# Kernel optimization log

Measured on AMD Instinct MI355X. Metric: run time of the kernel, lower is better.

## Reference

```python
import jax, jax.numpy as jnp
import numpy as np

D = 768
H = 8
HD = D // H  # 96
DFF = 2048
EPS = 1e-5


def layernorm(x, g, b):
    mu = jnp.mean(x, axis=-1, keepdims=True)
    var = jnp.var(x, axis=-1, keepdims=True)
    return (x - mu) * jax.lax.rsqrt(var + EPS) * g + b


def setup_inputs() -> dict:
    key = jax.random.key(0)
    ks = jax.random.split(key, 12)
    B, L = 4, 1024
    s = lambda fan: 1.0 / np.sqrt(fan)
    return {
        "x": jax.random.normal(ks[0], (B, L, D), jnp.float32),
        "attn_bias": jax.random.normal(ks[1], (B, L, L), jnp.float32),
        "in_proj_w": jax.random.normal(ks[2], (3 * D, D), jnp.float32) * s(D),
        "in_proj_b": jnp.zeros((3 * D,), jnp.float32),
        "out_w": jax.random.normal(ks[3], (D, D), jnp.float32) * s(D),
        "out_b": jnp.zeros((D,), jnp.float32),
        "ff1_w": jax.random.normal(ks[4], (DFF, D), jnp.float32) * s(D),
        "ff1_b": jnp.zeros((DFF,), jnp.float32),
        "ff2_w": jax.random.normal(ks[5], (D, DFF), jnp.float32) * s(DFF),
        "ff2_b": jnp.zeros((D,), jnp.float32),
        "ln1_g": jnp.ones((D,), jnp.float32),
        "ln1_b": jnp.zeros((D,), jnp.float32),
        "ln2_g": jnp.ones((D,), jnp.float32),
        "ln2_b": jnp.zeros((D,), jnp.float32),
    }


def reference(x, attn_bias, in_proj_w, in_proj_b, out_w, out_b,
              ff1_w, ff1_b, ff2_w, ff2_b, ln1_g, ln1_b, ln2_g, ln2_b):
    B, L, _ = x.shape
    # combined QKV projection (torch nn.MultiheadAttention in_proj)
    qkv = x @ in_proj_w.T + in_proj_b  # [B,L,3D]
    q, k, v = jnp.split(qkv, 3, axis=-1)
    q = q.reshape(B, L, H, HD).transpose(0, 2, 1, 3)  # [B,H,L,hd]
    k = k.reshape(B, L, H, HD).transpose(0, 2, 1, 3)
    v = v.reshape(B, L, H, HD).transpose(0, 2, 1, 3)
    scale = 1.0 / np.sqrt(HD)
    scores = jnp.einsum('bhld,bhmd->bhlm', q, k) * scale + attn_bias[:, None, :, :]
    probs = jax.nn.softmax(scores, axis=-1)
    attn = jnp.einsum('bhlm,bhmd->bhld', probs, v)  # [B,H,L,hd]
    attn = attn.transpose(0, 2, 1, 3).reshape(B, L, D)
    attn = attn @ out_w.T + out_b
    x = layernorm(x + attn, ln1_g, ln1_b)
    h = jax.nn.gelu(x @ ff1_w.T + ff1_b, approximate=False) @ ff2_w.T + ff2_b
    x = layernorm(x + h, ln2_g, ln2_b)
    return x
```

## Files before the change

kernel.cpp:

```cpp
#include <hip/hip_runtime.h>

typedef __bf16 bf16x8 __attribute__((ext_vector_type(8)));
typedef float f32x4 __attribute__((ext_vector_type(4)));
typedef unsigned short u16x8 __attribute__((ext_vector_type(8)));
typedef short s16x4 __attribute__((ext_vector_type(4)));

__device__ __forceinline__ unsigned short f2b(float f) {
    union { float f; unsigned u; } v; v.f = f;
    unsigned r = (v.u + 0x7fffu + ((v.u >> 16) & 1u)) >> 16;
    return (unsigned short)r;
}

__device__ __forceinline__ void load_lds16(const void* g, void* l) {
    __builtin_amdgcn_global_load_lds(
        (const __attribute__((address_space(1))) unsigned int*)g,
        (__attribute__((address_space(3))) unsigned int*)l,
        16, 0, 0);
}

__global__ void cvt_kernel(const float* __restrict__ in, unsigned short* __restrict__ out, int n4) {
    int i = blockIdx.x * 256 + threadIdx.x;
    if (i < n4) {
        f32x4 v = ((const f32x4*)in)[i];
        s16x4 o;
        o.x = (short)f2b(v.x);
        o.y = (short)f2b(v.y);
        o.z = (short)f2b(v.z);
        o.w = (short)f2b(v.w);
        ((s16x4*)out)[i] = o;
    }
}

template <int BM, int BN, int EPI>
__global__ __launch_bounds__(512, 1)
void gemm_pipe(const unsigned short* __restrict__ A, const unsigned short* __restrict__ Bm,
               const float* __restrict__ bias, void* __restrict__ Cout,
               int M, int N, int K) {
    constexpr int ACH = BM / 8;
    constexpr int TC  = (BM + BN) / 8;
    constexpr int CPW = TC / 8;
    constexpr int MR = 4;
    constexpr int NR = BN / 64;
    constexpr int WN = BN / 4;
    constexpr int WSTR = (WN == 64) ? 72 : 36;
    constexpr int ABYTES = BM * 128;
    constexpr int BBYTES = BN * 128;
    constexpr int SMEM_BYTES = 3 * (ABYTES + BBYTES);
    static_assert(8 * 64 * WSTR * 4 <= SMEM_BYTES, "epilogue fits");
    __shared__ char smem[SMEM_BYTES];

    const int tid = threadIdx.x, lane = tid & 63, wid = tid >> 6;
    const int l15 = lane & 15, lq = lane >> 4;
    const int wr = wid >> 2, wc = wid & 3;

    const int nwg = gridDim.x * gridDim.y;
    int bid = blockIdx.y * gridDim.x + blockIdx.x;
    bid = (bid & 7) * (nwg >> 3) + (bid >> 3);
    const int bx = bid % gridDim.x, by = bid / gridDim.x;
    const int m0 = by * BM, n0 = bx * BN;

    const int srow = lane >> 3;
    const int scol = ((lane & 7) ^ srow) * 8;

    f32x4 acc[MR][NR];
#pragma unroll
    for (int i = 0; i < MR; i++)
#pragma unroll
        for (int j = 0; j < NR; j++) acc[i][j] = 0.0f;

    auto stage = [&](int buf, int kt) {
        const int kb = kt * 64;
#pragma unroll
        for (int i = 0; i < CPW; ++i) {
            const int c = wid * CPW + i;
            if (c < ACH) {
                load_lds16(A + (size_t)(m0 + c * 8 + srow) * K + kb + scol,
                           smem + buf * ABYTES + c * 1024);
            } else {
                load_lds16(Bm + (size_t)(n0 + (c - ACH) * 8 + srow) * K + kb + scol,
                           smem + 3 * ABYTES + buf * BBYTES + (c - ACH) * 1024);
            }
        }
    };

    auto compute = [&](int buf) {
#pragma unroll
        for (int kc = 0; kc < 2; ++kc) {
            const int cb = kc * 64;
            const int sw = (l15 & 7) << 4;
            bf16x8 af[MR], bf[NR];
#pragma unroll
            for (int mi = 0; mi < MR; mi++) {
                const int row = wr * 64 + mi * 16 + l15;
                af[mi] = *(const bf16x8*)(smem + buf * ABYTES + row * 128 + ((cb + lq * 16) ^ sw));
            }
#pragma unroll
            for (int ni = 0; ni < NR; ni++) {
                const int row = wc * WN + ni * 16 + l15;
                bf[ni] = *(const bf16x8*)(smem + 3 * ABYTES + buf * BBYTES + row * 128 + ((cb + lq * 16) ^ sw));
            }
#pragma unroll
            for (int mi = 0; mi < MR; mi++)
#pragma unroll
                for (int ni = 0; ni < NR; ni++)
                    acc[mi][ni] = __builtin_amdgcn_mfma_f32_16x16x32_bf16(af[mi], bf[ni], acc[mi][ni], 0, 0, 0);
        }
    };

    const int nkt = K / 64;
    stage(0, 0);
    stage(1, 1);
    stage(2, 2);
    int cur = 0;
    for (int t = 0; t < nkt; ++t) {
        if (t <= nkt - 3)      asm volatile("s_waitcnt vmcnt(12)" ::: "memory");
        else if (t == nkt - 2) asm volatile("s_waitcnt vmcnt(6)" ::: "memory");
        else                   asm volatile("s_waitcnt vmcnt(0)" ::: "memory");
        __builtin_amdgcn_s_barrier();
        asm volatile("" ::: "memory");
        compute(cur);
        asm volatile("" ::: "memory");
        __builtin_amdgcn_s_barrier();
        if (t + 3 < nkt) stage(cur, t + 3);
        cur = (cur == 2) ? 0 : cur + 1;
    }

    float* ew = (float*)(smem + wid * 64 * WSTR * 4);
#pragma unroll
    for (int mi = 0; mi < MR; mi++) {
#pragma unroll
        for (int ni = 0; ni < NR; ni++) {
            const int cl = ni * 16 + l15;
            const float bv = bias[n0 + wc * WN + cl];
#pragma unroll
            for (int r = 0; r < 4; r++) {
                const int rl = mi * 16 + lq * 4 + r;
                float v = acc[mi][ni][r] + bv;
                if constexpr (EPI == 2) {
                    v = 0.5f * v * (1.0f + erff(v * 0.7071067811865475f));
                }
                ew[rl * WSTR + (cl ^ (lq << 3))] = v;
            }
        }
    }
    asm volatile("s_waitcnt lgkmcnt(0)" ::: "memory");

    if constexpr (WN == 64) {
        const int r8 = lane >> 3, c8 = lane & 7;
#pragma unroll
        for (int j = 0; j < 8; j++) {
            const int row = r8 + 8 * j;
            const int po = c8 ^ ((row >> 2) & 3);
            f32x4 a = *(const f32x4*)(ew + row * WSTR + po * 8);
            f32x4 b = *(const f32x4*)(ew + row * WSTR + po * 8 + 4);
            const int grow = m0 + wr * 64 + row;
            const int gcol = n0 + wc * WN + c8 * 8;
            if constexpr (EPI == 1) {
                *(f32x4*)&((float*)Cout)[(size_t)grow * N + gcol] = a;
                *(f32x4*)&((float*)Cout)[(size_t)grow * N + gcol + 4] = b;
            } else {
                u16x8 p;
#pragma unroll
                for (int e = 0; e < 4; e++) { p[e] = f2b(a[e]); p[e + 4] = f2b(b[e]); }
                *(u16x8*)&((unsigned short*)Cout)[(size_t)grow * N + gcol] = p;
            }
        }
    } else {
        const int r8 = lane >> 2, c8 = lane & 3;
#pragma unroll
        for (int j = 0; j < 4; j++) {
            const int row = r8 + 16 * j;
            const int po = c8 ^ ((row >> 2) & 3);
            f32x4 a = *(const f32x4*)(ew + row * WSTR + po * 8);
            f32x4 b = *(const f32x4*)(ew + row * WSTR + po * 8 + 4);
            const int grow = m0 + wr * 64 + row;
            const int gcol = n0 + wc * WN + c8 * 8;
            if constexpr (EPI == 1) {
                *(f32x4*)&((float*)Cout)[(size_t)grow * N + gcol] = a;
                *(f32x4*)&((float*)Cout)[(size_t)grow * N + gcol + 4] = b;
            } else {
                u16x8 p;
#pragma unroll
                for (int e = 0; e < 4; e++) { p[e] = f2b(a[e]); p[e + 4] = f2b(b[e]); }
                *(u16x8*)&((unsigned short*)Cout)[(size_t)grow * N + gcol] = p;
            }
        }
    }
}

__global__ __launch_bounds__(256, 2)
void attn_kernel(const unsigned short* __restrict__ qkv,
                 const float* __restrict__ bias,
                 unsigned short* __restrict__ out) {
    const int L = 1024, TD = 2304, HD = 96;
    const int qt = blockIdx.x, h = blockIdx.y, b = blockIdx.z;
    const int tid = threadIdx.x, lane = tid & 63, wid = tid >> 6;
    const int l15 = lane & 15, lq = lane >> 4;
    const int q0 = qt * 64;
    const float scale = 0.10206207261596576f;

    __shared__ unsigned short Ks[64][104];
    __shared__ unsigned short Vt[96][72];
    __shared__ unsigned short Ps[4][16][72];
    __shared__ float Ot[4][16][100];

    bf16x8 qf[3];
    const int qrow = q0 + wid * 16 + l15;
#pragma unroll
    for (int kc = 0; kc < 3; kc++)
        qf[kc] = *(const bf16x8*)(qkv + (size_t)(b * L + qrow) * TD + h * HD + kc * 32 + lq * 8);

    f32x4 o[6];
#pragma unroll
    for (int df = 0; df < 6; df++) o[df] = 0.0f;
    float mrow[4] = {-1e30f, -1e30f, -1e30f, -1e30f};
    float lrow[4] = {0.f, 0.f, 0.f, 0.f};

    for (int kv0 = 0; kv0 < L; kv0 += 64) {
#pragma unroll
        for (int i = 0; i < 3; i++) {
            int c = i * 256 + tid;
            int row = c / 12, cc = c % 12;
            *(f32x4*)&Ks[row][cc * 8] =
                *(const f32x4*)(qkv + (size_t)(b * L + kv0 + row) * TD + 768 + h * HD + cc * 8);
        }
#pragma unroll
        for (int i = 0; i < 3; i++) {
            int dblk = i * 4 + wid;
            int m = lane;
            u16x8 v = *(const u16x8*)(qkv + (size_t)(b * L + kv0 + m) * TD + 1536 + h * HD + dblk * 8);
#pragma unroll
            for (int j = 0; j < 8; j++) Vt[dblk * 8 + j][m] = v[j];
        }
        __syncthreads();

        f32x4 s[4];
#pragma unroll
        for (int nf = 0; nf < 4; nf++) s[nf] = 0.0f;
#pragma unroll
        for (int kc = 0; kc < 3; kc++) {
#pragma unroll
            for (int nf = 0; nf < 4; nf++) {
                bf16x8 kf = *(const bf16x8*)&Ks[nf * 16 + l15][kc * 32 + lq * 8];
                s[nf] = __builtin_amdgcn_mfma_f32_16x16x32_bf16(qf[kc], kf, s[nf], 0, 0, 0);
            }
        }
#pragma unroll
        for (int nf = 0; nf < 4; nf++) {
            int colg = kv0 + nf * 16 + l15;
#pragma unroll
            for (int r = 0; r < 4; r++) {
                int rowg = q0 + wid * 16 + lq * 4 + r;
                s[nf][r] = s[nf][r] * scale + bias[((size_t)b * L + rowg) * L + colg];
            }
        }
        float pm[4];
#pragma unroll
        for (int r = 0; r < 4; r++) {
            float mx = fmaxf(fmaxf(s[0][r], s[1][r]), fmaxf(s[2][r], s[3][r]));
#pragma unroll
            for (int d = 1; d < 16; d <<= 1) mx = fmaxf(mx, __shfl_xor(mx, d, 64));
            pm[r] = mx;
        }
        float alpha[4];
#pragma unroll
        for (int r = 0; r < 4; r++) {
            float mn = fmaxf(mrow[r], pm[r]);
            alpha[r] = __expf(mrow[r] - mn);
            mrow[r] = mn;
        }
        float rs[4] = {0.f, 0.f, 0.f, 0.f};
#pragma unroll
        for (int nf = 0; nf < 4; nf++)
#pragma unroll
            for (int r = 0; r < 4; r++) {
                float p = __expf(s[nf][r] - mrow[r]);
                s[nf][r] = p;
                rs[r] += p;
            }
#pragma unroll
        for (int r = 0; r < 4; r++) {
#pragma unroll
            for (int d = 1; d < 16; d <<= 1) rs[r] += __shfl_xor(rs[r], d, 64);
            lrow[r] = lrow[r] * alpha[r] + rs[r];
        }
#pragma unroll
        for (int nf = 0; nf < 4; nf++)
#pragma unroll
            for (int r = 0; r < 4; r++)
                Ps[wid][lq * 4 + r][nf * 16 + l15] = f2b(s[nf][r]);
#pragma unroll
        for (int df = 0; df < 6; df++)
#pragma unroll
            for (int r = 0; r < 4; r++) o[df][r] *= alpha[r];
        asm volatile("s_waitcnt lgkmcnt(0)" ::: "memory");
#pragma unroll
        for (int kc = 0; kc < 2; kc++) {
            bf16x8 pf = *(const bf16x8*)&Ps[wid][l15][kc * 32 + lq * 8];
#pragma unroll
            for (int df = 0; df < 6; df++) {
                bf16x8 vf = *(const bf16x8*)&Vt[df * 16 + l15][kc * 32 + lq * 8];
                o[df] = __builtin_amdgcn_mfma_f32_16x16x32_bf16(pf, vf, o[df], 0, 0, 0);
            }
        }
        __syncthreads();
    }

#pragma unroll
    for (int r = 0; r < 4; r++) {
        float inv = 1.0f / lrow[r];
        const int rl = lq * 4 + r;
#pragma unroll
        for (int df = 0; df < 6; df++) {
            const int cl = df * 16 + l15;
            Ot[wid][rl][cl ^ (lq << 3)] = o[df][r] * inv;
        }
    }
    asm volatile("s_waitcnt lgkmcnt(0)" ::: "memory");
    {
        const int r = lane >> 2, c8 = lane & 3;
        const int rowg = q0 + wid * 16 + r;
#pragma unroll
        for (int it = 0; it < 3; it++) {
            const int oc = c8 + 4 * it;
            const int po = oc ^ ((r >> 2) & 3);
            f32x4 a = *(const f32x4*)&Ot[wid][r][po * 8];
            f32x4 bb = *(const f32x4*)&Ot[wid][r][po * 8 + 4];
            u16x8 p;
#pragma unroll
            for (int e = 0; e < 4; e++) { p[e] = f2b(a[e]); p[e + 4] = f2b(bb[e]); }
            *(u16x8*)&out[((size_t)b * L + rowg) * 768 + h * 96 + oc * 8] = p;
        }
    }
}

template <int WRITE_B>
__global__ __launch_bounds__(256, 4)
void ln_kernel(const float* __restrict__ x, const float* __restrict__ res,
               const float* __restrict__ g, const float* __restrict__ bvec,
               float* __restrict__ outf, unsigned short* __restrict__ outb) {
    const int Dm = 768;
    int row = blockIdx.x;
    int tid = threadIdx.x;
    f32x4 v = {0.f, 0.f, 0.f, 0.f};
    float sum = 0.f, sq = 0.f;
    if (tid < 192) {
        f32x4 xv = ((const f32x4*)(x + (size_t)row * Dm))[tid];
        f32x4 rv = ((const f32x4*)(res + (size_t)row * Dm))[tid];
        v = xv + rv;
        sum = v.x + v.y + v.z + v.w;
        sq = v.x * v.x + v.y * v.y + v.z * v.z + v.w * v.w;
    }
#pragma unroll
    for (int d = 1; d < 64; d <<= 1) {
        sum += __shfl_xor(sum, d, 64);
        sq += __shfl_xor(sq, d, 64);
    }
    __shared__ float ps[8];
    int lane = tid & 63, wid = tid >> 6;
    if (lane == 0) { ps[wid] = sum; ps[wid + 4] = sq; }
    __syncthreads();
    sum = ps[0] + ps[1] + ps[2] + ps[3];
    sq = ps[4] + ps[5] + ps[6] + ps[7];
    float mu = sum * (1.0f / 768.0f);
    float var = sq * (1.0f / 768.0f) - mu * mu;
    float rsg = rsqrtf(var + 1e-5f);
    if (tid < 192) {
        f32x4 gv = ((const f32x4*)g)[tid];
        f32x4 bv = ((const f32x4*)bvec)[tid];
        f32x4 ov;
#pragma unroll
        for (int e = 0; e < 4; e++) ov[e] = (v[e] - mu) * rsg * gv[e] + bv[e];
        ((f32x4*)(outf + (size_t)row * Dm))[tid] = ov;
        if constexpr (WRITE_B) {
            s16x4 pb;
#pragma unroll
            for (int e = 0; e < 4; e++) pb[e] = (short)f2b(ov[e]);
            ((s16x4*)(outb + (size_t)row * Dm))[tid] = pb;
        }
    }
}

extern "C" void kernel_launch(void* const* d_in, const int* in_sizes, int n_in,
                              void* d_out, int out_size, void* d_ws, size_t ws_size,
                              hipStream_t stream) {
    (void)in_sizes; (void)n_in; (void)out_size; (void)ws_size;
    const float* x         = (const float*)d_in[0];
    const float* attn_bias = (const float*)d_in[1];
    const float* in_proj_w = (const float*)d_in[2];
    const float* in_proj_b = (const float*)d_in[3];
    const float* out_w     = (const float*)d_in[4];
    const float* out_b     = (const float*)d_in[5];
    const float* ff1_w     = (const float*)d_in[6];
    const float* ff1_b     = (const float*)d_in[7];
    const float* ff2_w     = (const float*)d_in[8];
    const float* ff2_b     = (const float*)d_in[9];
    const float* ln1_g     = (const float*)d_in[10];
    const float* ln1_b     = (const float*)d_in[11];
    const float* ln2_g     = (const float*)d_in[12];
    const float* ln2_b     = (const float*)d_in[13];

    const int NTOK = 4096;
    char* ws = (char*)d_ws;
    size_t off = 0;
    auto alloc = [&](size_t bytes) { void* p = ws + off; off += (bytes + 255) & ~(size_t)255; return p; };
    unsigned short* xb    = (unsigned short*)alloc((size_t)NTOK * 768 * 2);
    unsigned short* wqkv  = (unsigned short*)alloc((size_t)2304 * 768 * 2);
    unsigned short* wout  = (unsigned short*)alloc((size_t)768 * 768 * 2);
    unsigned short* wff1  = (unsigned short*)alloc((size_t)2048 * 768 * 2);
    unsigned short* wff2  = (unsigned short*)alloc((size_t)768 * 2048 * 2);
    unsigned short* qkvb  = (unsigned short*)alloc((size_t)NTOK * 2304 * 2);
    unsigned short* attnb = (unsigned short*)alloc((size_t)NTOK * 768 * 2);
    float*          aproj = (float*)alloc((size_t)NTOK * 768 * 4);
    float*          x1f   = (float*)alloc((size_t)NTOK * 768 * 4);
    unsigned short* x1b   = (unsigned short*)alloc((size_t)NTOK * 768 * 2);
    unsigned short* h1b  = qkvb;
    float*          ff2o = aproj;

    cvt_kernel<<<dim3((NTOK * 768 / 4) / 256), 256, 0, stream>>>(x, xb, NTOK * 768 / 4);
    cvt_kernel<<<dim3((2304 * 768 / 4) / 256), 256, 0, stream>>>(in_proj_w, wqkv, 2304 * 768 / 4);
    cvt_kernel<<<dim3((768 * 768 / 4) / 256), 256, 0, stream>>>(out_w, wout, 768 * 768 / 4);
    cvt_kernel<<<dim3((2048 * 768 / 4) / 256), 256, 0, stream>>>(ff1_w, wff1, 2048 * 768 / 4);
    cvt_kernel<<<dim3((768 * 2048 / 4) / 256), 256, 0, stream>>>(ff2_w, wff2, 768 * 2048 / 4);

    gemm_pipe<128, 256, 0><<<dim3(2304 / 256, NTOK / 128), 512, 0, stream>>>(xb, wqkv, in_proj_b, qkvb, NTOK, 2304, 768);
    attn_kernel<<<dim3(16, 8, 4), 256, 0, stream>>>(qkvb, attn_bias, attnb);
    gemm_pipe<128, 128, 1><<<dim3(768 / 128, NTOK / 128), 512, 0, stream>>>(attnb, wout, out_b, aproj, NTOK, 768, 768);
    ln_kernel<1><<<dim3(NTOK), 256, 0, stream>>>(x, aproj, ln1_g, ln1_b, x1f, x1b);
    gemm_pipe<128, 256, 2><<<dim3(2048 / 256, NTOK / 128), 512, 0, stream>>>(x1b, wff1, ff1_b, h1b, NTOK, 2048, 768);
    gemm_pipe<128, 128, 1><<<dim3(768 / 128, NTOK / 128), 512, 0, stream>>>(h1b, wff2, ff2_b, ff2o, NTOK, 768, 2048);
    ln_kernel<0><<<dim3(NTOK), 256, 0, stream>>>(x1f, ff2o, ln2_g, ln2_b, (float*)d_out, nullptr);
}
```

Before: 180.7 us.

## Interleave GEMM global-to-LDS staging with MFMA phases and fuse conversion kernels

Result: no change. 183.8 us (+1.7%).

```diff
diff --git a/kernel.cpp b/kernel.cpp
--- a/kernel.cpp
+++ b/kernel.cpp
@@ -18,30 +18,49 @@
         16, 0, 0);
 }
 
-__global__ void cvt_kernel(const float* __restrict__ in, unsigned short* __restrict__ out, int n4) {
+template <int N> __device__ __forceinline__ void wait_vmcnt() {
+    if constexpr (N == 0)      asm volatile("s_waitcnt vmcnt(0)" ::: "memory");
+    else if constexpr (N == 4) asm volatile("s_waitcnt vmcnt(4)" ::: "memory");
+    else if constexpr (N == 6) asm volatile("s_waitcnt vmcnt(6)" ::: "memory");
+    else static_assert(N == 0 || N == 4 || N == 6, "unsupported vmcnt");
+}
+
+__global__ void cvt5_kernel(const float* __restrict__ s0, const float* __restrict__ s1,
+                            const float* __restrict__ s2, const float* __restrict__ s3,
+                            const float* __restrict__ s4,
+                            unsigned short* __restrict__ d0, unsigned short* __restrict__ d1,
+                            unsigned short* __restrict__ d2, unsigned short* __restrict__ d3,
+                            unsigned short* __restrict__ d4) {
     int i = blockIdx.x * 256 + threadIdx.x;
-    if (i < n4) {
-        f32x4 v = ((const f32x4*)in)[i];
-        s16x4 o;
-        o.x = (short)f2b(v.x);
-        o.y = (short)f2b(v.y);
-        o.z = (short)f2b(v.z);
-        o.w = (short)f2b(v.w);
-        ((s16x4*)out)[i] = o;
-    }
-}
-
-template <int BM, int BN, int EPI>
+    const float* s; unsigned short* d; int off;
+    if (i < 786432)       { s = s0; d = d0; off = 0; }
+    else if (i < 1228800) { s = s1; d = d1; off = 786432; }
+    else if (i < 1376256) { s = s2; d = d2; off = 1228800; }
+    else if (i < 1769472) { s = s3; d = d3; off = 1376256; }
+    else                  { s = s4; d = d4; off = 1769472; }
+    i -= off;
+    f32x4 v = ((const f32x4*)s)[i];
+    s16x4 o;
+    o.x = (short)f2b(v.x);
+    o.y = (short)f2b(v.y);
+    o.z = (short)f2b(v.z);
+    o.w = (short)f2b(v.w);
+    ((s16x4*)d)[i] = o;
+}
+
+template <int BN, int EPI>
 __global__ __launch_bounds__(512, 1)
-void gemm_pipe(const unsigned short* __restrict__ A, const unsigned short* __restrict__ Bm,
-               const float* __restrict__ bias, void* __restrict__ Cout,
-               int M, int N, int K) {
+void gemm_8ph(const unsigned short* __restrict__ A, const unsigned short* __restrict__ Bm,
+              const float* __restrict__ bias, void* __restrict__ Cout,
+              int M, int N, int K) {
+    constexpr int BM = 128;
     constexpr int ACH = BM / 8;
-    constexpr int TC  = (BM + BN) / 8;
+    constexpr int BCH = BN / 8;
+    constexpr int TC  = ACH + BCH;
     constexpr int CPW = TC / 8;
-    constexpr int MR = 4;
-    constexpr int NR = BN / 64;
-    constexpr int WN = BN / 4;
+    constexpr int NR  = BN / 64;
+    constexpr int NPH = (BN == 256) ? 4 : 2;
+    constexpr int WN  = BN / 4;
     constexpr int WSTR = (WN == 64) ? 72 : 36;
     constexpr int ABYTES = BM * 128;
     constexpr int BBYTES = BN * 128;
@@ -52,6 +71,7 @@
     const int tid = threadIdx.x, lane = tid & 63, wid = tid >> 6;
     const int l15 = lane & 15, lq = lane >> 4;
     const int wr = wid >> 2, wc = wid & 3;
+    const int cw = wid * CPW;
 
     const int nwg = gridDim.x * gridDim.y;
     int bid = blockIdx.y * gridDim.x + blockIdx.x;
@@ -61,73 +81,92 @@
 
     const int srow = lane >> 3;
     const int scol = ((lane & 7) ^ srow) * 8;
-
-    f32x4 acc[MR][NR];
-#pragma unroll
-    for (int i = 0; i < MR; i++)
+    const int sw = (l15 & 7) << 4;
+
+    f32x4 acc[4][NR];
+#pragma unroll
+    for (int i = 0; i < 4; i++)
 #pragma unroll
         for (int j = 0; j < NR; j++) acc[i][j] = 0.0f;
 
-    auto stage = [&](int buf, int kt) {
+    auto stage_chunk = [&](int buf, int kt, int c) {
         const int kb = kt * 64;
-#pragma unroll
-        for (int i = 0; i < CPW; ++i) {
-            const int c = wid * CPW + i;
-            if (c < ACH) {
-                load_lds16(A + (size_t)(m0 + c * 8 + srow) * K + kb + scol,
-                           smem + buf * ABYTES + c * 1024);
-            } else {
-                load_lds16(Bm + (size_t)(n0 + (c - ACH) * 8 + srow) * K + kb + scol,
-                           smem + 3 * ABYTES + buf * BBYTES + (c - ACH) * 1024);
-            }
+        if (c < ACH) {
+            load_lds16(A + (size_t)(m0 + c * 8 + srow) * K + kb + scol,
+                       smem + buf * ABYTES + c * 1024);
+        } else {
+            load_lds16(Bm + (size_t)(n0 + (c - ACH) * 8 + srow) * K + kb + scol,
+                       smem + 3 * ABYTES + buf * BBYTES + (c - ACH) * 1024);
         }
     };
 
-    auto compute = [&](int buf) {
-#pragma unroll
-        for (int kc = 0; kc < 2; ++kc) {
+    const int nkt = K / 64;
+#pragma unroll
+    for (int i = 0; i < CPW; ++i) stage_chunk(0, 0, cw + i);
+#pragma unroll
+    for (int i = 0; i < CPW; ++i) stage_chunk(1, 1, cw + i);
+    wait_vmcnt<CPW>();
+    __builtin_amdgcn_s_barrier();
+
+    for (int t = 0; t < nkt; ++t) {
+        const int buf = t % 3;
+        const int sb = (t + 2 < nkt) ? ((t + 2) % 3) : 0;
+        const bool do_stage = (t + 2) < nkt;
+        const char* Ab = smem + buf * ABYTES;
+        const char* Bb = smem + 3 * ABYTES + buf * BBYTES;
+        bf16x8 af[4];
+#pragma unroll
+        for (int ph = 0; ph < NPH; ++ph) {
+            const int kc = (NPH == 4) ? (ph >> 1) : ph;
+            const int nh = (NPH == 4) ? (ph & 1) : 0;
             const int cb = kc * 64;
-            const int sw = (l15 & 7) << 4;
-            bf16x8 af[MR], bf[NR];
-#pragma unroll
-            for (int mi = 0; mi < MR; mi++) {
-                const int row = wr * 64 + mi * 16 + l15;
-                af[mi] = *(const bf16x8*)(smem + buf * ABYTES + row * 128 + ((cb + lq * 16) ^ sw));
-            }
-#pragma unroll
-            for (int ni = 0; ni < NR; ni++) {
+            if (nh == 0) {
+#pragma unroll
+                for (int mi = 0; mi < 4; mi++) {
+                    const int row = wr * 64 + mi * 16 + l15;
+                    af[mi] = *(const bf16x8*)(Ab + row * 128 + ((cb + lq * 16) ^ sw));
+                }
+            }
+            bf16x8 bfp[2];
+#pragma unroll
+            for (int j = 0; j < 2; j++) {
+                const int ni = nh * 2 + j;
                 const int row = wc * WN + ni * 16 + l15;
-                bf[ni] = *(const bf16x8*)(smem + 3 * ABYTES + buf * BBYTES + row * 128 + ((cb + lq * 16) ^ sw));
-            }
-#pragma unroll
-            for (int mi = 0; mi < MR; mi++)
-#pragma unroll
-                for (int ni = 0; ni < NR; ni++)
-                    acc[mi][ni] = __builtin_amdgcn_mfma_f32_16x16x32_bf16(af[mi], bf[ni], acc[mi][ni], 0, 0, 0);
-        }
-    };
-
-    const int nkt = K / 64;
-    stage(0, 0);
-    stage(1, 1);
-    stage(2, 2);
-    int cur = 0;
-    for (int t = 0; t < nkt; ++t) {
-        if (t <= nkt - 3)      asm volatile("s_waitcnt vmcnt(12)" ::: "memory");
-        else if (t == nkt - 2) asm volatile("s_waitcnt vmcnt(6)" ::: "memory");
-        else                   asm volatile("s_waitcnt vmcnt(0)" ::: "memory");
-        __builtin_amdgcn_s_barrier();
-        asm volatile("" ::: "memory");
-        compute(cur);
-        asm volatile("" ::: "memory");
-        __builtin_amdgcn_s_barrier();
-        if (t + 3 < nkt) stage(cur, t + 3);
-        cur = (cur == 2) ? 0 : cur + 1;
+                bfp[j] = *(const bf16x8*)(Bb + row * 128 + ((cb + lq * 16) ^ sw));
+            }
+            if (do_stage) {
+                if (NPH == 4) {
+                    if (ph == 0)      { stage_chunk(sb, t + 2, cw + 0); stage_chunk(sb, t + 2, cw + 1); }
+                    else if (ph == 1) { stage_chunk(sb, t + 2, cw + 2); stage_chunk(sb, t + 2, cw + 3); }
+                    else if (ph == 2) { stage_chunk(sb, t + 2, cw + 4); }
+                    else              { stage_chunk(sb, t + 2, cw + 5); }
+                } else {
+                    if (ph == 0)      { stage_chunk(sb, t + 2, cw + 0); stage_chunk(sb, t + 2, cw + 1); }
+                    else              { stage_chunk(sb, t + 2, cw + 2); stage_chunk(sb, t + 2, cw + 3); }
+                }
+            }
+            __builtin_amdgcn_s_barrier();
+            asm volatile("s_waitcnt lgkmcnt(0)" ::: "memory");
+            __builtin_amdgcn_sched_barrier(0);
+            __builtin_amdgcn_s_setprio(1);
+#pragma unroll
+            for (int mi = 0; mi < 4; mi++)
+#pragma unroll
+                for (int j = 0; j < 2; j++) {
+                    const int ni = nh * 2 + j;
+                    acc[mi][ni] = __builtin_amdgcn_mfma_f32_16x16x32_bf16(af[mi], bfp[j], acc[mi][ni], 0, 0, 0);
+                }
+            __builtin_amdgcn_s_setprio(0);
+            if (ph == NPH - 1) {
+                if (do_stage) wait_vmcnt<CPW>(); else wait_vmcnt<0>();
+            }
+            __builtin_amdgcn_s_barrier();
+        }
     }
 
     float* ew = (float*)(smem + wid * 64 * WSTR * 4);
 #pragma unroll
-    for (int mi = 0; mi < MR; mi++) {
+    for (int mi = 0; mi < 4; mi++) {
 #pragma unroll
         for (int ni = 0; ni < NR; ni++) {
             const int cl = ni * 16 + l15;
@@ -417,17 +456,14 @@
     unsigned short* h1b  = qkvb;
     float*          ff2o = aproj;
 
-    cvt_kernel<<<dim3((NTOK * 768 / 4) / 256), 256, 0, stream>>>(x, xb, NTOK * 768 / 4);
-    cvt_kernel<<<dim3((2304 * 768 / 4) / 256), 256, 0, stream>>>(in_proj_w, wqkv, 2304 * 768 / 4);
-    cvt_kernel<<<dim3((768 * 768 / 4) / 256), 256, 0, stream>>>(out_w, wout, 768 * 768 / 4);
-    cvt_kernel<<<dim3((2048 * 768 / 4) / 256), 256, 0, stream>>>(ff1_w, wff1, 2048 * 768 / 4);
-    cvt_kernel<<<dim3((768 * 2048 / 4) / 256), 256, 0, stream>>>(ff2_w, wff2, 768 * 2048 / 4);
-
-    gemm_pipe<128, 256, 0><<<dim3(2304 / 256, NTOK / 128), 512, 0, stream>>>(xb, wqkv, in_proj_b, qkvb, NTOK, 2304, 768);
+    cvt5_kernel<<<dim3(8448), 256, 0, stream>>>(x, in_proj_w, out_w, ff1_w, ff2_w,
+                                                xb, wqkv, wout, wff1, wff2);
+
+    gemm_8ph<256, 0><<<dim3(2304 / 256, NTOK / 128), 512, 0, stream>>>(xb, wqkv, in_proj_b, qkvb, NTOK, 2304, 768);
     attn_kernel<<<dim3(16, 8, 4), 256, 0, stream>>>(qkvb, attn_bias, attnb);
-    gemm_pipe<128, 128, 1><<<dim3(768 / 128, NTOK / 128), 512, 0, stream>>>(attnb, wout, out_b, aproj, NTOK, 768, 768);
+    gemm_8ph<128, 1><<<dim3(768 / 128, NTOK / 128), 512, 0, stream>>>(attnb, wout, out_b, aproj, NTOK, 768, 768);
     ln_kernel<1><<<dim3(NTOK), 256, 0, stream>>>(x, aproj, ln1_g, ln1_b, x1f, x1b);
-    gemm_pipe<128, 256, 2><<<dim3(2048 / 256, NTOK / 128), 512, 0, stream>>>(x1b, wff1, ff1_b, h1b, NTOK, 2048, 768);
-    gemm_pipe<128, 128, 1><<<dim3(768 / 128, NTOK / 128), 512, 0, stream>>>(h1b, wff2, ff2_b, ff2o, NTOK, 768, 2048);
+    gemm_8ph<256, 2><<<dim3(2048 / 256, NTOK / 128), 512, 0, stream>>>(x1b, wff1, ff1_b, h1b, NTOK, 2048, 768);
+    gemm_8ph<128, 1><<<dim3(768 / 128, NTOK / 128), 512, 0, stream>>>(h1b, wff2, ff2_b, ff2o, NTOK, 768, 2048);
     ln_kernel<0><<<dim3(NTOK), 256, 0, stream>>>(x1f, ff2o, ln2_g, ln2_b, (float*)d_out, nullptr);
 }
```
